# Kernel tuning notes

Hardware: AMD Instinct MI355X
Metric: run time of the kernel (lower is better)

Reference implementation:

```python
import jax, jax.numpy as jnp
import numpy as np

B, L_MAX, D, RL, RD, DOUT = 64, 4096, 128, 64, 16, 512
LN_EPS = 1e-5

def _xavier(key, shape):
    fan_in, fan_out = shape[0], shape[1]
    limit = np.sqrt(6.0 / (fan_in + fan_out)).astype(np.float32)
    return jax.random.uniform(key, shape, jnp.float32, -limit, limit)

def setup_inputs() -> dict:
    key = jax.random.key(0)
    ks = jax.random.split(key, 10)
    emb = jax.random.normal(ks[0], (B, L_MAX, D), jnp.float32)
    # contiguous padding mask from random true lengths (standard ESM padding)
    lengths = jax.random.randint(ks[1], (B,), 1, L_MAX + 1)
    mask = (jnp.arange(L_MAX)[None, :] < lengths[:, None])  # bool [B, L_max]
    B_c = _xavier(ks[2], (D, RD))
    A_c = _xavier(ks[3], (L_MAX, RL))
    H_c = _xavier(ks[4], (RL * RD, DOUT))
    W1 = _xavier(ks[5], (DOUT, DOUT))
    b1 = jnp.zeros((DOUT,), jnp.float32)
    ln_w = jnp.ones((DOUT,), jnp.float32)
    ln_b = jnp.zeros((DOUT,), jnp.float32)
    W2 = _xavier(ks[6], (DOUT, DOUT))
    b2 = jnp.zeros((DOUT,), jnp.float32)
    return {"emb": emb, "mask": mask, "B_c": B_c, "A_c": A_c, "H_c": H_c,
            "W1": W1, "b1": b1, "ln_w": ln_w, "ln_b": ln_b, "W2": W2, "b2": b2}

def reference(emb, mask, B_c, A_c, H_c, W1, b1, ln_w, ln_b, W2, b2):
    m = mask.astype(emb.dtype)                      # [B, L]
    X = emb * m[:, :, None]                         # masked embeddings [B, L, D]
    Y = jnp.einsum('bld,dr->blr', X, B_c)           # low-rank proj over D -> [B, L, rD]
    U = jnp.einsum('blr,lk->bkr', Y, A_c)           # low-rank proj over L -> [B, rL, rD]
    z = U.reshape(U.shape[0], -1) @ H_c             # [B, d]
    # expander: Linear -> LayerNorm -> ReLU -> Linear
    h = z @ W1 + b1
    mu = jnp.mean(h, axis=-1, keepdims=True)
    var = jnp.mean(jnp.square(h - mu), axis=-1, keepdims=True)
    h = (h - mu) / jnp.sqrt(var + LN_EPS) * ln_w + ln_b
    h = jax.nn.relu(h)
    return h @ W2 + b2
```

## Files before the change

### kernel.cpp

```cpp
#include <hip/hip_runtime.h>


__global__ __launch_bounds__(256) void detect_mask(
    const unsigned int* __restrict__ m, int* __restrict__ flag)
{
    unsigned int v = 0;
    int base = (blockIdx.x * 256 + threadIdx.x) * 4;
#pragma unroll
    for (int i = 0; i < 4; ++i) v |= m[base + i];
    unsigned long long any = __ballot(v > 1u);
    if ((threadIdx.x & 63) == 0 && any) atomicOr(flag, 1);
}

#define YS_STRIDE 20
#define BCS_CHUNK 516
__global__ __launch_bounds__(256, 4) void k1_proj(
    const float* __restrict__ emb,
    const void* __restrict__ maskp,
    const float* __restrict__ Bc,
    const float* __restrict__ Ac,
    float* __restrict__ Part,
    const int* __restrict__ flag)
{
    __shared__ __align__(16) float BcS[4 * BCS_CHUNK];
    __shared__ __align__(16) float As[64 * 64];
    __shared__ __align__(16) float Ys[64 * YS_STRIDE];

    const int tid  = threadIdx.x;
    const int lane = tid & 63;
    const int wave = tid >> 6;
    const int q    = tid & 3;
    const int r    = tid >> 2;
    const int b    = blockIdx.x >> 4;
    const int c    = blockIdx.x & 15;
    const int byte_mode = *flag;

#pragma unroll
    for (int i = 0; i < 8; ++i) {
        int e = i * 256 + tid;
        int k = e >> 4, col = e & 15;
        BcS[(k >> 5) * BCS_CHUNK + (k & 31) * 16 + col] = Bc[e];
    }
    __syncthreads();

    float accU[4] = {0.f, 0.f, 0.f, 0.f};

    for (int t = 0; t < 4; ++t) {
        const long l0 = (long)c * 256 + t * 64;
        const float* asrc = Ac + l0 * 64;

#pragma unroll
        for (int i = 0; i < 4; ++i) {
            int e = (i * 256 + tid) * 4;
            *(float4*)(As + e) = *(const float4*)(asrc + e);
        }

        const float* xrow = emb + ((long)b * 4096 + l0 + r) * 128 + q * 32;
        float4 xv[8];
#pragma unroll
        for (int j = 0; j < 8; ++j) xv[j] = *(const float4*)(xrow + j * 4);

        const float* bq = BcS + q * BCS_CHUNK;
        float y[16];
#pragma unroll
        for (int j = 0; j < 16; ++j) y[j] = 0.f;
#pragma unroll
        for (int j4 = 0; j4 < 8; ++j4) {
            float4 v = xv[j4];
#pragma unroll
            for (int i = 0; i < 4; ++i) {
                int kk = j4 * 4 + i;
                float x = (i == 0) ? v.x : (i == 1) ? v.y : (i == 2) ? v.z : v.w;
#pragma unroll
                for (int c4 = 0; c4 < 4; ++c4) {
                    float4 bv = *(const float4*)(bq + kk * 16 + c4 * 4);
                    y[c4 * 4 + 0] += x * bv.x;
                    y[c4 * 4 + 1] += x * bv.y;
                    y[c4 * 4 + 2] += x * bv.z;
                    y[c4 * 4 + 3] += x * bv.w;
                }
            }
        }
#pragma unroll
        for (int j = 0; j < 16; ++j) {
            y[j] += __shfl_xor(y[j], 1);
            y[j] += __shfl_xor(y[j], 2);
        }

        long midx = (long)b * 4096 + l0 + r;
        bool mb = byte_mode ? (((const unsigned char*)maskp)[midx] != 0)
                            : (((const int*)maskp)[midx] != 0);
        float mv = mb ? 1.f : 0.f;
        float4 yo;
        if (q == 0)      yo = make_float4(y[0],  y[1],  y[2],  y[3]);
        else if (q == 1) yo = make_float4(y[4],  y[5],  y[6],  y[7]);
        else if (q == 2) yo = make_float4(y[8],  y[9],  y[10], y[11]);
        else             yo = make_float4(y[12], y[13], y[14], y[15]);
        yo.x *= mv; yo.y *= mv; yo.z *= mv; yo.w *= mv;
        *(float4*)(Ys + r * YS_STRIDE + q * 4) = yo;
        __syncthreads();

        for (int l = 0; l < 64; ++l) {
            float av = As[l * 64 + lane];
            float4 yv = *(const float4*)(Ys + l * YS_STRIDE + wave * 4);
            accU[0] += av * yv.x; accU[1] += av * yv.y;
            accU[2] += av * yv.z; accU[3] += av * yv.w;
        }
        __syncthreads();
    }

    float4 uo = {accU[0], accU[1], accU[2], accU[3]};
    *(float4*)(Part + ((long)(c * 64 + b)) * 1024 + lane * 16 + wave * 4) = uo;
}

__global__ __launch_bounds__(256) void k2a(
    const float* __restrict__ Part,
    const float* __restrict__ Hc,
    float* __restrict__ zbuf)
{
    __shared__ __align__(16) float Us[1024];
    __shared__ __align__(16) float hp[8][128];

    const int tid = threadIdx.x;
    const int b   = blockIdx.x >> 2;
    const int jq  = blockIdx.x & 3;

    {
        const float* pb = Part + (long)b * 1024 + tid * 4;
        float4 s = {0.f, 0.f, 0.f, 0.f};
#pragma unroll
        for (int cc = 0; cc < 16; ++cc) {
            float4 v = *(const float4*)(pb + (long)cc * 64 * 1024);
            s.x += v.x; s.y += v.y; s.z += v.z; s.w += v.w;
        }
        *(float4*)(Us + tid * 4) = s;
    }
    __syncthreads();

    const int c4 = (tid & 31) * 4;
    const int kq = tid >> 5;
    const int k0 = kq * 128;
    float a0 = 0.f, a1 = 0.f, a2 = 0.f, a3 = 0.f;
    for (int k4 = 0; k4 < 128; k4 += 4) {
        float4 u = *(const float4*)(Us + k0 + k4);
        const float* hcp = Hc + (long)(k0 + k4) * 512 + jq * 128 + c4;
        float4 w0  = *(const float4*)(hcp);
        float4 w1v = *(const float4*)(hcp + 512);
        float4 w2v = *(const float4*)(hcp + 1024);
        float4 w3  = *(const float4*)(hcp + 1536);
        a0 += u.x * w0.x + u.y * w1v.x + u.z * w2v.x + u.w * w3.x;
        a1 += u.x * w0.y + u.y * w1v.y + u.z * w2v.y + u.w * w3.y;
        a2 += u.x * w0.z + u.y * w1v.z + u.z * w2v.z + u.w * w3.z;
        a3 += u.x * w0.w + u.y * w1v.w + u.z * w2v.w + u.w * w3.w;
    }
    float4 p = {a0, a1, a2, a3};
    *(float4*)(&hp[kq][c4]) = p;
    __syncthreads();

    if (tid < 128) {
        float z = hp[0][tid] + hp[1][tid] + hp[2][tid] + hp[3][tid]
                + hp[4][tid] + hp[5][tid] + hp[6][tid] + hp[7][tid];
        zbuf[(long)b * 512 + jq * 128 + tid] = z;
    }
}

__global__ __launch_bounds__(256) void k2b(
    const float* __restrict__ zbuf,
    const float* __restrict__ W1,
    const float* __restrict__ b1,
    float* __restrict__ gbuf,
    float* __restrict__ pstat)
{
    __shared__ __align__(16) float zs[512];
    __shared__ __align__(16) float hp[8][128];
    __shared__ float red[8];

    const int tid = threadIdx.x;
    const int b   = blockIdx.x >> 2;
    const int jq  = blockIdx.x & 3;

    if (tid < 128)
        *(float4*)(zs + tid * 4) = *(const float4*)(zbuf + (long)b * 512 + tid * 4);
    __syncthreads();

    const int c4 = (tid & 31) * 4;
    const int kq = tid >> 5;
    const int k0 = kq * 64;
    float a0 = 0.f, a1 = 0.f, a2 = 0.f, a3 = 0.f;
    for (int k4 = 0; k4 < 64; k4 += 4) {
        float4 u = *(const float4*)(zs + k0 + k4);
        const float* wp = W1 + (long)(k0 + k4) * 512 + jq * 128 + c4;
        float4 w0  = *(const float4*)(wp);
        float4 w1v = *(const float4*)(wp + 512);
        float4 w2v = *(const float4*)(wp + 1024);
        float4 w3  = *(const float4*)(wp + 1536);
        a0 += u.x * w0.x + u.y * w1v.x + u.z * w2v.x + u.w * w3.x;
        a1 += u.x * w0.y + u.y * w1v.y + u.z * w2v.y + u.w * w3.y;
        a2 += u.x * w0.z + u.y * w1v.z + u.z * w2v.z + u.w * w3.z;
        a3 += u.x * w0.w + u.y * w1v.w + u.z * w2v.w + u.w * w3.w;
    }
    float4 p = {a0, a1, a2, a3};
    *(float4*)(&hp[kq][c4]) = p;
    __syncthreads();

    float s = 0.f, s2 = 0.f;
    if (tid < 128) {
        float hv = hp[0][tid] + hp[1][tid] + hp[2][tid] + hp[3][tid]
                 + hp[4][tid] + hp[5][tid] + hp[6][tid] + hp[7][tid]
                 + b1[jq * 128 + tid];
        gbuf[(long)b * 512 + jq * 128 + tid] = hv;
        s = hv; s2 = hv * hv;
    }
#pragma unroll
    for (int m = 32; m >= 1; m >>= 1) {
        s  += __shfl_xor(s, m);
        s2 += __shfl_xor(s2, m);
    }
    const int wave = tid >> 6, lane = tid & 63;
    if (lane == 0) { red[wave] = s; red[wave + 4] = s2; }
    __syncthreads();
    if (tid == 0) {
        pstat[((long)b * 4 + jq) * 2 + 0] = red[0] + red[1] + red[2] + red[3];
        pstat[((long)b * 4 + jq) * 2 + 1] = red[4] + red[5] + red[6] + red[7];
    }
}

__global__ __launch_bounds__(256) void k2c(
    const float* __restrict__ gbuf,
    const float* __restrict__ pstat,
    const float* __restrict__ lnw,
    const float* __restrict__ lnb,
    const float* __restrict__ W2,
    const float* __restrict__ b2,
    float* __restrict__ out)
{
    __shared__ __align__(16) float hs[512];
    __shared__ __align__(16) float hp[8][128];

    const int tid = threadIdx.x;
    const int b   = blockIdx.x >> 2;
    const int jq  = blockIdx.x & 3;

    float S = 0.f, S2 = 0.f;
#pragma unroll
    for (int qq = 0; qq < 4; ++qq) {
        S  += pstat[((long)b * 4 + qq) * 2 + 0];
        S2 += pstat[((long)b * 4 + qq) * 2 + 1];
    }
    const float mu   = S * (1.f / 512.f);
    const float var  = S2 * (1.f / 512.f) - mu * mu;
    const float rstd = rsqrtf(var + 1e-5f);

    if (tid < 128) {
        float4 g  = *(const float4*)(gbuf + (long)b * 512 + tid * 4);
        float4 w  = *(const float4*)(lnw + tid * 4);
        float4 bb = *(const float4*)(lnb + tid * 4);
        float h0 = (g.x - mu) * rstd * w.x + bb.x;
        float h1 = (g.y - mu) * rstd * w.y + bb.y;
        float h2 = (g.z - mu) * rstd * w.z + bb.z;
        float h3 = (g.w - mu) * rstd * w.w + bb.w;
        h0 = h0 > 0.f ? h0 : 0.f;
        h1 = h1 > 0.f ? h1 : 0.f;
        h2 = h2 > 0.f ? h2 : 0.f;
        h3 = h3 > 0.f ? h3 : 0.f;
        *(float4*)(hs + tid * 4) = make_float4(h0, h1, h2, h3);
    }
    __syncthreads();

    const int c4 = (tid & 31) * 4;
    const int kq = tid >> 5;
    const int k0 = kq * 64;
    float a0 = 0.f, a1 = 0.f, a2 = 0.f, a3 = 0.f;
    for (int k4 = 0; k4 < 64; k4 += 4) {
        float4 u = *(const float4*)(hs + k0 + k4);
        const float* wp = W2 + (long)(k0 + k4) * 512 + jq * 128 + c4;
        float4 w0  = *(const float4*)(wp);
        float4 w1v = *(const float4*)(wp + 512);
        float4 w2v = *(const float4*)(wp + 1024);
        float4 w3  = *(const float4*)(wp + 1536);
        a0 += u.x * w0.x + u.y * w1v.x + u.z * w2v.x + u.w * w3.x;
        a1 += u.x * w0.y + u.y * w1v.y + u.z * w2v.y + u.w * w3.y;
        a2 += u.x * w0.z + u.y * w1v.z + u.z * w2v.z + u.w * w3.z;
        a3 += u.x * w0.w + u.y * w1v.w + u.z * w2v.w + u.w * w3.w;
    }
    float4 p = {a0, a1, a2, a3};
    *(float4*)(&hp[kq][c4]) = p;
    __syncthreads();

    if (tid < 128) {
        float o = hp[0][tid] + hp[1][tid] + hp[2][tid] + hp[3][tid]
                + hp[4][tid] + hp[5][tid] + hp[6][tid] + hp[7][tid]
                + b2[jq * 128 + tid];
        out[(long)b * 512 + jq * 128 + tid] = o;
    }
}

extern "C" void kernel_launch(void* const* d_in, const int* in_sizes, int n_in,
                              void* d_out, int out_size, void* d_ws, size_t ws_size,
                              hipStream_t stream) {
    const float* emb = (const float*)d_in[0];
    const void*  msk = (const void*)d_in[1];
    const float* Bc  = (const float*)d_in[2];
    const float* Ac  = (const float*)d_in[3];
    const float* Hc  = (const float*)d_in[4];
    const float* W1  = (const float*)d_in[5];
    const float* b1  = (const float*)d_in[6];
    const float* lnw = (const float*)d_in[7];
    const float* lnb = (const float*)d_in[8];
    const float* W2  = (const float*)d_in[9];
    const float* b2  = (const float*)d_in[10];

    float* Part  = (float*)d_ws;
    int*   flg   = (int*)((char*)d_ws + 4 * 1024 * 1024);
    float* zbuf  = (float*)((char*)d_ws + 4 * 1024 * 1024 + 4096);
    float* gbuf  = zbuf + 64 * 512;
    float* pstat = gbuf + 64 * 512;

    hipMemsetAsync(flg, 0, 4, stream);
    detect_mask<<<64, 256, 0, stream>>>((const unsigned int*)msk, flg);
    k1_proj<<<1024, 256, 0, stream>>>(emb, msk, Bc, Ac, Part, flg);
    k2a<<<256, 256, 0, stream>>>(Part, Hc, zbuf);
    k2b<<<256, 256, 0, stream>>>(zbuf, W1, b1, gbuf, pstat);
    k2c<<<256, 256, 0, stream>>>(gbuf, pstat, lnw, lnb, W2, b2, (float*)d_out);
}
```

Measured before the change: 260.7 us.

## Split fused projection kernel into separate Y and U kernels via global workspace

```diff
diff --git a/kernel.cpp b/kernel.cpp
--- a/kernel.cpp
+++ b/kernel.cpp
@@ -12,27 +12,22 @@
     if ((threadIdx.x & 63) == 0 && any) atomicOr(flag, 1);
 }
 
-#define YS_STRIDE 20
 #define BCS_CHUNK 516
-__global__ __launch_bounds__(256, 4) void k1_proj(
+__global__ __launch_bounds__(256, 3) void y_proj(
     const float* __restrict__ emb,
     const void* __restrict__ maskp,
     const float* __restrict__ Bc,
-    const float* __restrict__ Ac,
-    float* __restrict__ Part,
+    float* __restrict__ Y,
     const int* __restrict__ flag)
 {
     __shared__ __align__(16) float BcS[4 * BCS_CHUNK];
-    __shared__ __align__(16) float As[64 * 64];
-    __shared__ __align__(16) float Ys[64 * YS_STRIDE];
-
-    const int tid  = threadIdx.x;
-    const int lane = tid & 63;
-    const int wave = tid >> 6;
-    const int q    = tid & 3;
-    const int r    = tid >> 2;
-    const int b    = blockIdx.x >> 4;
-    const int c    = blockIdx.x & 15;
+
+    const int tid = threadIdx.x;
+    const int q   = tid & 3;
+    const int r2  = tid >> 2;
+    const int b   = blockIdx.x >> 5;
+    const int rg  = blockIdx.x & 31;
+    const long l0 = (long)rg * 128;
     const int byte_mode = *flag;
 
 #pragma unroll
@@ -43,74 +38,122 @@
     }
     __syncthreads();
 
-    float accU[4] = {0.f, 0.f, 0.f, 0.f};
-
-    for (int t = 0; t < 4; ++t) {
-        const long l0 = (long)c * 256 + t * 64;
-        const float* asrc = Ac + l0 * 64;
-
+    const long row0 = (long)b * 4096 + l0 + r2;
+    const long row1 = row0 + 64;
+    const float* x0p = emb + row0 * 128 + q * 32;
+    const float* x1p = emb + row1 * 128 + q * 32;
+    float4 xv0[8], xv1[8];
+#pragma unroll
+    for (int j = 0; j < 8; ++j) xv0[j] = *(const float4*)(x0p + j * 4);
+#pragma unroll
+    for (int j = 0; j < 8; ++j) xv1[j] = *(const float4*)(x1p + j * 4);
+
+    const float* bq = BcS + q * BCS_CHUNK;
+    float y0[16], y1[16];
+#pragma unroll
+    for (int j = 0; j < 16; ++j) { y0[j] = 0.f; y1[j] = 0.f; }
+#pragma unroll
+    for (int j4 = 0; j4 < 8; ++j4) {
+        float4 v0 = xv0[j4], v1 = xv1[j4];
 #pragma unroll
         for (int i = 0; i < 4; ++i) {
-            int e = (i * 256 + tid) * 4;
-            *(float4*)(As + e) = *(const float4*)(asrc + e);
-        }
-
-        const float* xrow = emb + ((long)b * 4096 + l0 + r) * 128 + q * 32;
-        float4 xv[8];
-#pragma unroll
-        for (int j = 0; j < 8; ++j) xv[j] = *(const float4*)(xrow + j * 4);
-
-        const float* bq = BcS + q * BCS_CHUNK;
-        float y[16];
-#pragma unroll
-        for (int j = 0; j < 16; ++j) y[j] = 0.f;
-#pragma unroll
-        for (int j4 = 0; j4 < 8; ++j4) {
-            float4 v = xv[j4];
-#pragma unroll
-            for (int i = 0; i < 4; ++i) {
-                int kk = j4 * 4 + i;
-                float x = (i == 0) ? v.x : (i == 1) ? v.y : (i == 2) ? v.z : v.w;
-#pragma unroll
-                for (int c4 = 0; c4 < 4; ++c4) {
-                    float4 bv = *(const float4*)(bq + kk * 16 + c4 * 4);
-                    y[c4 * 4 + 0] += x * bv.x;
-                    y[c4 * 4 + 1] += x * bv.y;
-                    y[c4 * 4 + 2] += x * bv.z;
-                    y[c4 * 4 + 3] += x * bv.w;
-                }
+            int kk = j4 * 4 + i;
+            float xa = (i == 0) ? v0.x : (i == 1) ? v0.y : (i == 2) ? v0.z : v0.w;
+            float xb = (i == 0) ? v1.x : (i == 1) ? v1.y : (i == 2) ? v1.z : v1.w;
+#pragma unroll
+            for (int c4 = 0; c4 < 4; ++c4) {
+                float4 bv = *(const float4*)(bq + kk * 16 + c4 * 4);
+                y0[c4 * 4 + 0] += xa * bv.x; y0[c4 * 4 + 1] += xa * bv.y;
+                y0[c4 * 4 + 2] += xa * bv.z; y0[c4 * 4 + 3] += xa * bv.w;
+                y1[c4 * 4 + 0] += xb * bv.x; y1[c4 * 4 + 1] += xb * bv.y;
+                y1[c4 * 4 + 2] += xb * bv.z; y1[c4 * 4 + 3] += xb * bv.w;
             }
         }
-#pragma unroll
-        for (int j = 0; j < 16; ++j) {
-            y[j] += __shfl_xor(y[j], 1);
-            y[j] += __shfl_xor(y[j], 2);
-        }
-
-        long midx = (long)b * 4096 + l0 + r;
-        bool mb = byte_mode ? (((const unsigned char*)maskp)[midx] != 0)
-                            : (((const int*)maskp)[midx] != 0);
-        float mv = mb ? 1.f : 0.f;
-        float4 yo;
-        if (q == 0)      yo = make_float4(y[0],  y[1],  y[2],  y[3]);
-        else if (q == 1) yo = make_float4(y[4],  y[5],  y[6],  y[7]);
-        else if (q == 2) yo = make_float4(y[8],  y[9],  y[10], y[11]);
-        else             yo = make_float4(y[12], y[13], y[14], y[15]);
-        yo.x *= mv; yo.y *= mv; yo.z *= mv; yo.w *= mv;
-        *(float4*)(Ys + r * YS_STRIDE + q * 4) = yo;
-        __syncthreads();
-
-        for (int l = 0; l < 64; ++l) {
-            float av = As[l * 64 + lane];
-            float4 yv = *(const float4*)(Ys + l * YS_STRIDE + wave * 4);
-            accU[0] += av * yv.x; accU[1] += av * yv.y;
-            accU[2] += av * yv.z; accU[3] += av * yv.w;
-        }
-        __syncthreads();
-    }
-
-    float4 uo = {accU[0], accU[1], accU[2], accU[3]};
-    *(float4*)(Part + ((long)(c * 64 + b)) * 1024 + lane * 16 + wave * 4) = uo;
+    }
+#pragma unroll
+    for (int j = 0; j < 16; ++j) {
+        y0[j] += __shfl_xor(y0[j], 1); y0[j] += __shfl_xor(y0[j], 2);
+        y1[j] += __shfl_xor(y1[j], 1); y1[j] += __shfl_xor(y1[j], 2);
+    }
+
+    bool mb0 = byte_mode ? (((const unsigned char*)maskp)[row0] != 0)
+                         : (((const int*)maskp)[row0] != 0);
+    bool mb1 = byte_mode ? (((const unsigned char*)maskp)[row1] != 0)
+                         : (((const int*)maskp)[row1] != 0);
+    float m0 = mb0 ? 1.f : 0.f, m1 = mb1 ? 1.f : 0.f;
+
+    float4 o0, o1;
+    if (q == 0)      { o0 = make_float4(y0[0],y0[1],y0[2],y0[3]);
+                       o1 = make_float4(y1[0],y1[1],y1[2],y1[3]); }
+    else if (q == 1) { o0 = make_float4(y0[4],y0[5],y0[6],y0[7]);
+                       o1 = make_float4(y1[4],y1[5],y1[6],y1[7]); }
+    else if (q == 2) { o0 = make_float4(y0[8],y0[9],y0[10],y0[11]);
+                       o1 = make_float4(y1[8],y1[9],y1[10],y1[11]); }
+    else             { o0 = make_float4(y0[12],y0[13],y0[14],y0[15]);
+                       o1 = make_float4(y1[12],y1[13],y1[14],y1[15]); }
+    o0.x *= m0; o0.y *= m0; o0.z *= m0; o0.w *= m0;
+    o1.x *= m1; o1.y *= m1; o1.z *= m1; o1.w *= m1;
+    *(float4*)(Y + row0 * 16 + q * 4) = o0;
+    *(float4*)(Y + row1 * 16 + q * 4) = o1;
+}
+
+__global__ __launch_bounds__(256) void u_part(
+    const float* __restrict__ Ac,
+    const float* __restrict__ Y,
+    float* __restrict__ Part)
+{
+    __shared__ __align__(16) float Lred[4 * 64 * 16];
+
+    const int tid = threadIdx.x;
+    const int cg  = tid & 3;
+    const int kg  = (tid >> 2) & 15;
+    const int ls  = tid >> 6;
+    const int b   = blockIdx.x >> 4;
+    const int c   = blockIdx.x & 15;
+    const long l0 = (long)c * 256 + ls * 64;
+
+    const float* ap = Ac + l0 * 64 + kg * 4;
+    const float* yp = Y + ((long)b * 4096 + l0) * 16 + cg * 4;
+
+    float acc[4][4];
+#pragma unroll
+    for (int i = 0; i < 4; ++i)
+#pragma unroll
+        for (int j = 0; j < 4; ++j) acc[i][j] = 0.f;
+
+#pragma unroll 8
+    for (int l = 0; l < 64; ++l) {
+        float4 a4 = *(const float4*)(ap + l * 64);
+        float4 y4 = *(const float4*)(yp + l * 16);
+        acc[0][0] += a4.x * y4.x; acc[0][1] += a4.x * y4.y;
+        acc[0][2] += a4.x * y4.z; acc[0][3] += a4.x * y4.w;
+        acc[1][0] += a4.y * y4.x; acc[1][1] += a4.y * y4.y;
+        acc[1][2] += a4.y * y4.z; acc[1][3] += a4.y * y4.w;
+        acc[2][0] += a4.z * y4.x; acc[2][1] += a4.z * y4.y;
+        acc[2][2] += a4.z * y4.z; acc[2][3] += a4.z * y4.w;
+        acc[3][0] += a4.w * y4.x; acc[3][1] += a4.w * y4.y;
+        acc[3][2] += a4.w * y4.z; acc[3][3] += a4.w * y4.w;
+    }
+
+#pragma unroll
+    for (int i = 0; i < 4; ++i) {
+        float4 p = {acc[i][0], acc[i][1], acc[i][2], acc[i][3]};
+        *(float4*)(&Lred[ls * 1024 + (kg * 4 + i) * 16 + cg * 4]) = p;
+    }
+    __syncthreads();
+
+    const int k  = tid >> 2;
+    const int cq = tid & 3;
+    float4 s0 = *(const float4*)(&Lred[0 * 1024 + k * 16 + cq * 4]);
+    float4 s1 = *(const float4*)(&Lred[1 * 1024 + k * 16 + cq * 4]);
+    float4 s2 = *(const float4*)(&Lred[2 * 1024 + k * 16 + cq * 4]);
+    float4 s3 = *(const float4*)(&Lred[3 * 1024 + k * 16 + cq * 4]);
+    float4 s;
+    s.x = s0.x + s1.x + s2.x + s3.x;
+    s.y = s0.y + s1.y + s2.y + s3.y;
+    s.z = s0.z + s1.z + s2.z + s3.z;
+    s.w = s0.w + s1.w + s2.w + s3.w;
+    *(float4*)(Part + ((long)(c * 64 + b)) * 1024 + k * 16 + cq * 4) = s;
 }
 
 __global__ __launch_bounds__(256) void k2a(
@@ -310,15 +353,17 @@
     const float* W2  = (const float*)d_in[9];
     const float* b2  = (const float*)d_in[10];
 
-    float* Part  = (float*)d_ws;
-    int*   flg   = (int*)((char*)d_ws + 4 * 1024 * 1024);
-    float* zbuf  = (float*)((char*)d_ws + 4 * 1024 * 1024 + 4096);
+    float* Yw    = (float*)d_ws;
+    float* Part  = Yw + (long)64 * 4096 * 16;
+    int*   flg   = (int*)(Part + 16 * 64 * 1024);
+    float* zbuf  = (float*)((char*)flg + 4096);
     float* gbuf  = zbuf + 64 * 512;
     float* pstat = gbuf + 64 * 512;
 
     hipMemsetAsync(flg, 0, 4, stream);
     detect_mask<<<64, 256, 0, stream>>>((const unsigned int*)msk, flg);
-    k1_proj<<<1024, 256, 0, stream>>>(emb, msk, Bc, Ac, Part, flg);
+    y_proj<<<2048, 256, 0, stream>>>(emb, msk, Bc, Yw, flg);
+    u_part<<<1024, 256, 0, stream>>>(Ac, Yw, Part);
     k2a<<<256, 256, 0, stream>>>(Part, Hc, zbuf);
     k2b<<<256, 256, 0, stream>>>(zbuf, W1, b1, gbuf, pstat);
     k2c<<<256, 256, 0, stream>>>(gbuf, pstat, lnw, lnb, W2, b2, (float*)d_out);
```

Measured after the change: 303.4 us. 16.4% more time.
